# Kernel tuning notes

Measured on AMD Instinct MI355X. Metric: run time of the kernel, lower is better.

Reference implementation:

```python
import jax, jax.numpy as jnp
import numpy as np

N_HOPS = 6
NEG_INF = -1e30


def setup_inputs() -> dict:
    key = jax.random.key(0)
    ks = jax.random.split(key, 12)
    B, L, T, V, D, C = 64, 512, 8, 50000, 1024, 3
    context_ids = jax.random.randint(ks[0], (B, L), 0, V, dtype=jnp.int32)
    target_ids = jax.random.randint(ks[1], (B, T), 0, V, dtype=jnp.int32)
    context_len = jax.random.randint(ks[2], (B,), 256, L + 1, dtype=jnp.int32)
    target_len = jax.random.randint(ks[3], (B,), 2, T + 1, dtype=jnp.int32)
    target_offset = jax.random.randint(ks[4], (B,), 0, 256, dtype=jnp.int32)
    s = 0.02
    return {
        "context_ids": context_ids,
        "target_ids": target_ids,
        "context_len": context_len,
        "target_len": target_len,
        "target_offset": target_offset,
        "embedding_matrix": jax.random.normal(ks[5], (V, D), jnp.float32) * s,
        "W_lin": jax.random.normal(ks[6], (D, D), jnp.float32) * s,
        "b_lin": jax.random.normal(ks[7], (D,), jnp.float32) * s,
        "w_attn": jax.random.normal(ks[8], (2 * D, 1), jnp.float32) * s,
        "b_attn": jax.random.normal(ks[9], (1,), jnp.float32) * s,
        "W_out": jax.random.normal(ks[10], (D, C), jnp.float32) * s,
        "b_out": jax.random.normal(ks[11], (C,), jnp.float32) * s,
    }


def reference(context_ids, target_ids, context_len, target_len, target_offset,
              embedding_matrix, W_lin, b_lin, w_attn, b_attn, W_out, b_out):
    B, L = context_ids.shape
    T = target_ids.shape[1]

    pos = jnp.arange(L, dtype=jnp.int32)[None, :]            # [1,L]
    ctx_mask = pos < context_len[:, None]                    # [B,L] valid positions

    # location model 2: v_i = 1 - |i - target_offset| / seq_len, zeroed off-sequence
    dist = jnp.abs(pos - target_offset[:, None]).astype(jnp.float32)
    v_loc = (1.0 - dist / context_len[:, None].astype(jnp.float32))
    v_loc = jnp.where(ctx_mask, v_loc, 0.0)                  # [B,L]

    memory = embedding_matrix[context_ids]                   # [B,L,D]
    ext_memory = memory * v_loc[..., None]                   # [B,L,D] (loc-model-2 branch)

    # v_aspect: variable-length mean of target embeddings
    tgt_emb = embedding_matrix[target_ids]                   # [B,T,D]
    t_mask = (jnp.arange(T, dtype=jnp.int32)[None, :] < target_len[:, None])
    v_aspect = (tgt_emb * t_mask[..., None].astype(jnp.float32)).sum(axis=1)
    v_aspect = v_aspect / target_len[:, None].astype(jnp.float32)  # [B,D]

    vec = v_aspect
    for _ in range(N_HOPS):  # fixed hop count; linear + attn params shared (AUTO_REUSE)
        lin = vec @ W_lin + b_lin                            # [B,D]
        # content attention: tanh(W [m_i ; v] + b) scores
        s_mem = jnp.einsum('bld,dk->bl', ext_memory, w_attn[: ext_memory.shape[-1]])
        s_vec = vec @ w_attn[ext_memory.shape[-1]:]          # [B,1]
        scores = jnp.tanh(s_mem + s_vec + b_attn[0])         # [B,L]
        scores = jnp.where(ctx_mask, scores, NEG_INF)
        alpha = jax.nn.softmax(scores, axis=-1)              # [B,L]
        attn_out = jnp.einsum('bl,bld->bd', alpha, ext_memory)
        vec = attn_out + lin

    logits = vec @ W_out + b_out                             # [B,C]
    return logits
```

## Files before the change

kernel.cpp:

```cpp
#include <hip/hip_runtime.h>
#include <cstdint>


#define DD 1024
#define LL 512
#define BB 64
#define MTS 32

__global__ __launch_bounds__(256) void k_init(const float* __restrict__ w_attn,
                                              const float* __restrict__ W_out,
                                              float* __restrict__ Mt,
                                              float* __restrict__ Mc)
{
  int d = blockIdx.x * 256 + threadIdx.x;
  float w0 = w_attn[d];
  float u0 = w_attn[DD + d];
  Mt[d * MTS + 0] = w0; Mc[0 * DD + d] = w0;
  Mt[d * MTS + 1] = u0; Mc[1 * DD + d] = u0;
#pragma unroll
  for (int c = 0; c < 3; ++c) {
    float y = W_out[d * 3 + c];
    int col = 7 + 6 * c;
    Mt[d * MTS + col] = y; Mc[col * DD + d] = y;
  }
}

__global__ __launch_bounds__(256) void k_chain(const float* __restrict__ Wl,
                                               float* __restrict__ Mt,
                                               float* __restrict__ Mc,
                                               int i0, int i1, int i2, int i3,
                                               int o0, int o1, int o2, int o3)
{
  int tid = threadIdx.x;
  int wv = __builtin_amdgcn_readfirstlane(tid >> 6);
  int ln = tid & 63;
  int i = blockIdx.x * 4 + wv;
  const float* wrow = Wl + (size_t)i * DD;
  int c0 = i0 < 0 ? 0 : i0, c1 = i1 < 0 ? 0 : i1;
  int c2 = i2 < 0 ? 0 : i2, c3 = i3 < 0 ? 0 : i3;
  float s0 = 0.f, s1 = 0.f, s2 = 0.f, s3 = 0.f;
  for (int m = 0; m < 16; ++m) {
    int j = ln + m * 64;
    float w = wrow[j];
    s0 += w * Mc[c0 * DD + j];
    s1 += w * Mc[c1 * DD + j];
    s2 += w * Mc[c2 * DD + j];
    s3 += w * Mc[c3 * DD + j];
  }
#pragma unroll
  for (int m = 1; m < 64; m <<= 1) {
    s0 += __shfl_xor(s0, m, 64); s1 += __shfl_xor(s1, m, 64);
    s2 += __shfl_xor(s2, m, 64); s3 += __shfl_xor(s3, m, 64);
  }
  if (ln == 0) {
    if (o0 >= 0) { Mt[i * MTS + o0] = s0; Mc[o0 * DD + i] = s0; }
    if (o1 >= 0) { Mt[i * MTS + o1] = s1; Mc[o1 * DD + i] = s1; }
    if (o2 >= 0) { Mt[i * MTS + o2] = s2; Mc[o2 * DD + i] = s2; }
    if (o3 >= 0) { Mt[i * MTS + o3] = s3; Mc[o3 * DD + i] = s3; }
  }
}

__global__ __launch_bounds__(256, 2) void k_gemm(const int* __restrict__ ctx_ids,
                                                 const int* __restrict__ ctx_len,
                                                 const int* __restrict__ toff,
                                                 const float* __restrict__ emb,
                                                 const float* __restrict__ Mt,
                                                 float* __restrict__ Q)
{
  __shared__ float stag[4][64 * 33];
  __shared__ float qp[4][64][25];
  int tid = threadIdx.x;
  int kq = __builtin_amdgcn_readfirstlane(tid >> 6);
  int ln = tid & 63;
  int rowbase = blockIdx.x * 64;
  int myid = ctx_ids[rowbase + ln];
  const float* base[8];
#pragma unroll
  for (int ii = 0; ii < 8; ++ii) {
    int rid = __shfl(myid, ii * 8 + (ln >> 3), 64);
    base[ii] = emb + (size_t)rid * DD;
  }
  int p4 = (ln & 7) * 4;
  float* sw = stag[kq];
  int k0 = kq * 256;
  float acc[25];
#pragma unroll
  for (int j = 0; j < 25; ++j) acc[j] = 0.f;

  float4 buf[8];
#pragma unroll
  for (int ii = 0; ii < 8; ++ii)
    buf[ii] = *(const float4*)(base[ii] + k0 + p4);

  for (int ch = 0; ch < 8; ++ch) {
#pragma unroll
    for (int ii = 0; ii < 8; ++ii) {
      int r = ii * 8 + (ln >> 3);
      int a = r * 33 + p4;
      sw[a + 0] = buf[ii].x; sw[a + 1] = buf[ii].y;
      sw[a + 2] = buf[ii].z; sw[a + 3] = buf[ii].w;
    }
    if (ch < 7) {
      int kb = k0 + (ch + 1) * 32;
#pragma unroll
      for (int ii = 0; ii < 8; ++ii)
        buf[ii] = *(const float4*)(base[ii] + kb + p4);
    }
    __builtin_amdgcn_s_waitcnt(0xc07f);
    const float* mrow = Mt + (size_t)(k0 + ch * 32) * MTS;
#pragma unroll 4
    for (int kk = 0; kk < 32; ++kk) {
      float mv = sw[ln * 33 + kk];
#pragma unroll
      for (int j = 0; j < 25; ++j) acc[j] += mv * mrow[kk * MTS + j];
    }
  }
#pragma unroll
  for (int j = 0; j < 25; ++j) qp[kq][ln][j] = acc[j];
  __syncthreads();

  int b = rowbase >> 9;
  int l0 = rowbase & 511;
  int clen = ctx_len[b];
  int off = toff[b];
  float fclen = (float)clen;
  for (int i = tid; i < 1600; i += 256) {
    int j = i >> 6, r = i & 63;
    float s = qp[0][r][j] + qp[1][r][j] + qp[2][r][j] + qp[3][r][j];
    int l = l0 + r;
    float vl = (l < clen) ? (1.f - fabsf((float)(l - off)) / fclen) : 0.f;
    Q[((size_t)b * 25 + j) * LL + l] = s * vl;
  }
}

template <bool ISMAX>
__device__ __forceinline__ void breduce(float* v, int n, float* lds, int tid)
{
  int wv = __builtin_amdgcn_readfirstlane(tid >> 6);
  int ln = tid & 63;
  for (int q = 0; q < n; ++q) {
    float x = v[q];
#pragma unroll
    for (int m = 1; m < 64; m <<= 1) {
      float o = __shfl_xor(x, m, 64);
      x = ISMAX ? fmaxf(x, o) : x + o;
    }
    if (ln == 0) lds[q * 4 + wv] = x;
  }
  __syncthreads();
  for (int q = 0; q < n; ++q) {
    float a = lds[q * 4 + 0], b = lds[q * 4 + 1];
    float c = lds[q * 4 + 2], d = lds[q * 4 + 3];
    v[q] = ISMAX ? fmaxf(fmaxf(a, b), fmaxf(c, d)) : ((a + b) + (c + d));
  }
  __syncthreads();
}

__global__ __launch_bounds__(256) void k_hop(const int* __restrict__ tgt_ids,
                                             const int* __restrict__ tgt_len,
                                             const int* __restrict__ ctx_len,
                                             const float* __restrict__ emb,
                                             const float* __restrict__ b_lin,
                                             const float* __restrict__ b_attn,
                                             const float* __restrict__ b_out,
                                             const float* __restrict__ Mc,
                                             const float* __restrict__ Q,
                                             float* __restrict__ out)
{
  __shared__ float Qs[25 * LL];
  __shared__ float va[DD];
  __shared__ float red[36 * 4];
  int tid = threadIdx.x;
  int b = blockIdx.x;

  for (int i = tid; i < 25 * LL; i += 256) Qs[i] = Q[(size_t)b * (25 * LL) + i];

  int tl = tgt_len[b];
  float inv_tl = 1.f / (float)tl;
  for (int d = tid; d < DD; d += 256) {
    float s = 0.f;
#pragma unroll
    for (int t = 0; t < 8; ++t)
      if (t < tl) s += emb[(size_t)tgt_ids[b * 8 + t] * DD + d];
    va[d] = s * inv_tl;
  }
  __syncthreads();

  float p[32];
#pragma unroll
  for (int q = 0; q < 32; ++q) p[q] = 0.f;
  for (int d = tid; d < DD; d += 256) {
    float vad = va[d], bd = b_lin[d];
#pragma unroll
    for (int k = 0; k < 6; ++k) {
      float u = Mc[(1 + k) * DD + d];
      p[k] += vad * u;
      if (k < 5) p[9 + k] += bd * u;
    }
#pragma unroll
    for (int c = 0; c < 3; ++c) {
      p[6 + c] += vad * Mc[(25 + c) * DD + d];
#pragma unroll
      for (int k = 0; k < 6; ++k)
        p[14 + c * 6 + k] += bd * Mc[(7 + 6 * c + k) * DD + d];
    }
  }
  breduce<false>(p, 32, red, tid);

  float tcur[6], rc[3], beta[5], gam[18];
#pragma unroll
  for (int k = 0; k < 6; ++k) tcur[k] = p[k];
#pragma unroll
  for (int c = 0; c < 3; ++c) rc[c] = p[6 + c];
#pragma unroll
  for (int k = 0; k < 5; ++k) beta[k] = p[9 + k];
#pragma unroll
  for (int q = 0; q < 18; ++q) gam[q] = p[14 + q];

  int clen = ctx_len[b];
  float batt = b_attn[0];
  int l1 = tid, l2 = tid + 256;

  for (int h = 0; h < 6; ++h) {
    float s_h = tcur[0];
    float sc1 = -1e30f, sc2 = -1e30f;
    if (l1 < clen) sc1 = tanhf(Qs[l1] + s_h + batt);
    if (l2 < clen) sc2 = tanhf(Qs[l2] + s_h + batt);
    float mx = fmaxf(sc1, sc2);
    breduce<true>(&mx, 1, red, tid);

    float pe[9];
#pragma unroll
    for (int q = 0; q < 9; ++q) pe[q] = 0.f;
    int kd = 5 - h;
    if (l1 < clen) {
      float e = expf(sc1 - mx);
      pe[0] += e;
      for (int k = 0; k <= 4 - h; ++k) pe[1 + k] += e * Qs[(1 + k) * LL + l1];
#pragma unroll
      for (int c = 0; c < 3; ++c) pe[6 + c] += e * Qs[(7 + 6 * c + kd) * LL + l1];
    }
    if (l2 < clen) {
      float e = expf(sc2 - mx);
      pe[0] += e;
      for (int k = 0; k <= 4 - h; ++k) pe[1 + k] += e * Qs[(1 + k) * LL + l2];
#pragma unroll
      for (int c = 0; c < 3; ++c) pe[6 + c] += e * Qs[(7 + 6 * c + kd) * LL + l2];
    }
    breduce<false>(pe, 9, red, tid);

    float invS = 1.f / pe[0];
    for (int k = 0; k <= 4 - h; ++k)
      tcur[k] = pe[1 + k] * invS + tcur[k + 1] + beta[k];
#pragma unroll
    for (int c = 0; c < 3; ++c)
      rc[c] = pe[6 + c] * invS + rc[c] + gam[c * 6 + kd];
  }
  if (tid < 3) out[b * 3 + tid] = rc[tid] + b_out[tid];
}

extern "C" void kernel_launch(void* const* d_in, const int* in_sizes, int n_in,
                              void* d_out, int out_size, void* d_ws, size_t ws_size,
                              hipStream_t stream)
{
  const int*   ctx_ids = (const int*)d_in[0];
  const int*   tgt_ids = (const int*)d_in[1];
  const int*   ctx_len = (const int*)d_in[2];
  const int*   tgt_len = (const int*)d_in[3];
  const int*   toff    = (const int*)d_in[4];
  const float* emb     = (const float*)d_in[5];
  const float* Wl      = (const float*)d_in[6];
  const float* bl      = (const float*)d_in[7];
  const float* wat     = (const float*)d_in[8];
  const float* bat     = (const float*)d_in[9];
  const float* Wo      = (const float*)d_in[10];
  const float* bo      = (const float*)d_in[11];
  float* ws = (float*)d_ws;
  float* Mt = ws;
  float* Mc = ws + 32768;
  float* Q  = ws + 65536;
  float* outp = (float*)d_out;

  hipLaunchKernelGGL(k_init, dim3(4), dim3(256), 0, stream, wat, Wo, Mt, Mc);
  for (int s = 1; s <= 6; ++s) {
    int i0 = (s <= 5) ? s : -1;
    int o0 = (s <= 5) ? (1 + s) : -1;
    int i1 = 6 + s,  o1 = (s <= 5) ? (7 + s)  : 25;
    int i2 = 12 + s, o2 = (s <= 5) ? (13 + s) : 26;
    int i3 = 18 + s, o3 = (s <= 5) ? (19 + s) : 27;
    hipLaunchKernelGGL(k_chain, dim3(256), dim3(256), 0, stream,
                       Wl, Mt, Mc, i0, i1, i2, i3, o0, o1, o2, o3);
  }
  hipLaunchKernelGGL(k_gemm, dim3(512), dim3(256), 0, stream,
                     ctx_ids, ctx_len, toff, emb, Mt, Q);
  hipLaunchKernelGGL(k_hop, dim3(64), dim3(256), 0, stream,
                     tgt_ids, tgt_len, ctx_len, emb, bl, bat, bo, Mc, Q, outp);
}
```

Measured before the change: 363.4 us.

## Fuse init and chain launches into one cooperative kernel with grid syncs

Replaces the init kernel and six chained matvec launches with a single cooperative kernel that uses grid.sync between chain steps and keeps each W_lin row in registers across all steps. The target-embedding mean and the per-batch projection dot products move into this kernel, so the hop kernel only loads a 32-value vector per batch. The hop kernel now uses 512 threads, one per position, with float4 staging of Q into shared memory. This removes several launch gaps and repeated W_lin reads, at the cost of grid-wide barrier overhead and a dependence on cooperative launch support.

```diff
diff --git a/kernel.cpp b/kernel.cpp
--- a/kernel.cpp
+++ b/kernel.cpp
@@ -1,5 +1,8 @@
 #include <hip/hip_runtime.h>
+#include <hip/hip_cooperative_groups.h>
 #include <cstdint>
+
+namespace cg = cooperative_groups;
 
 
 #define DD 1024
@@ -7,56 +10,134 @@
 #define BB 64
 #define MTS 32
 
-__global__ __launch_bounds__(256) void k_init(const float* __restrict__ w_attn,
-                                              const float* __restrict__ W_out,
-                                              float* __restrict__ Mt,
-                                              float* __restrict__ Mc)
-{
-  int d = blockIdx.x * 256 + threadIdx.x;
-  float w0 = w_attn[d];
-  float u0 = w_attn[DD + d];
-  Mt[d * MTS + 0] = w0; Mc[0 * DD + d] = w0;
-  Mt[d * MTS + 1] = u0; Mc[1 * DD + d] = u0;
-#pragma unroll
-  for (int c = 0; c < 3; ++c) {
-    float y = W_out[d * 3 + c];
-    int col = 7 + 6 * c;
-    Mt[d * MTS + col] = y; Mc[col * DD + d] = y;
-  }
-}
-
-__global__ __launch_bounds__(256) void k_chain(const float* __restrict__ Wl,
-                                               float* __restrict__ Mt,
-                                               float* __restrict__ Mc,
-                                               int i0, int i1, int i2, int i3,
-                                               int o0, int o1, int o2, int o3)
-{
-  int tid = threadIdx.x;
+template <bool ISMAX, int NW>
+__device__ __forceinline__ void breduce(float* v, int n, float* lds, int tid)
+{
   int wv = __builtin_amdgcn_readfirstlane(tid >> 6);
   int ln = tid & 63;
-  int i = blockIdx.x * 4 + wv;
+  for (int q = 0; q < n; ++q) {
+    float x = v[q];
+#pragma unroll
+    for (int m = 1; m < 64; m <<= 1) {
+      float o = __shfl_xor(x, m, 64);
+      x = ISMAX ? fmaxf(x, o) : x + o;
+    }
+    if (ln == 0) lds[q * NW + wv] = x;
+  }
+  __syncthreads();
+  for (int q = 0; q < n; ++q) {
+    float r = lds[q * NW + 0];
+#pragma unroll
+    for (int w = 1; w < NW; ++w)
+      r = ISMAX ? fmaxf(r, lds[q * NW + w]) : r + lds[q * NW + w];
+    v[q] = r;
+  }
+  __syncthreads();
+}
+
+__global__ __launch_bounds__(256) void k_prep(const int* __restrict__ tgt_ids,
+                                              const int* __restrict__ tgt_len,
+                                              const float* __restrict__ emb,
+                                              const float* __restrict__ Wl,
+                                              const float* __restrict__ bl,
+                                              const float* __restrict__ wat,
+                                              const float* __restrict__ Wo,
+                                              float* __restrict__ Mt,
+                                              float* __restrict__ Mc,
+                                              float* __restrict__ va_ws,
+                                              float* __restrict__ pv)
+{
+  cg::grid_group grid = cg::this_grid();
+  __shared__ float red[32 * 4];
+  int tid = threadIdx.x;
+  int blk = blockIdx.x;
+  int gidx = blk * 256 + tid;
+
+  if (gidx < DD) {
+    int d = gidx;
+    float w0 = wat[d];
+    float u0 = wat[DD + d];
+    Mt[d * MTS + 0] = w0; Mc[0 * DD + d] = w0;
+    Mt[d * MTS + 1] = u0; Mc[1 * DD + d] = u0;
+#pragma unroll
+    for (int c = 0; c < 3; ++c) {
+      float y = Wo[d * 3 + c];
+      int col = 7 + 6 * c;
+      Mt[d * MTS + col] = y; Mc[col * DD + d] = y;
+    }
+  }
+  {
+    int b = gidx >> 10, d = gidx & (DD - 1);
+    int tl = tgt_len[b];
+    float s = 0.f;
+#pragma unroll
+    for (int t = 0; t < 8; ++t)
+      if (t < tl) s += emb[(size_t)tgt_ids[b * 8 + t] * DD + d];
+    va_ws[gidx] = s / (float)tl;
+  }
+  grid.sync();
+
+  int wv = tid >> 6, ln = tid & 63;
+  int i = blk * 4 + wv;
   const float* wrow = Wl + (size_t)i * DD;
-  int c0 = i0 < 0 ? 0 : i0, c1 = i1 < 0 ? 0 : i1;
-  int c2 = i2 < 0 ? 0 : i2, c3 = i3 < 0 ? 0 : i3;
-  float s0 = 0.f, s1 = 0.f, s2 = 0.f, s3 = 0.f;
-  for (int m = 0; m < 16; ++m) {
-    int j = ln + m * 64;
-    float w = wrow[j];
-    s0 += w * Mc[c0 * DD + j];
-    s1 += w * Mc[c1 * DD + j];
-    s2 += w * Mc[c2 * DD + j];
-    s3 += w * Mc[c3 * DD + j];
-  }
-#pragma unroll
-  for (int m = 1; m < 64; m <<= 1) {
-    s0 += __shfl_xor(s0, m, 64); s1 += __shfl_xor(s1, m, 64);
-    s2 += __shfl_xor(s2, m, 64); s3 += __shfl_xor(s3, m, 64);
-  }
-  if (ln == 0) {
-    if (o0 >= 0) { Mt[i * MTS + o0] = s0; Mc[o0 * DD + i] = s0; }
-    if (o1 >= 0) { Mt[i * MTS + o1] = s1; Mc[o1 * DD + i] = s1; }
-    if (o2 >= 0) { Mt[i * MTS + o2] = s2; Mc[o2 * DD + i] = s2; }
-    if (o3 >= 0) { Mt[i * MTS + o3] = s3; Mc[o3 * DD + i] = s3; }
+  float wreg[16];
+#pragma unroll
+  for (int m = 0; m < 16; ++m) wreg[m] = wrow[ln + m * 64];
+
+  for (int s = 1; s <= 6; ++s) {
+    int c0 = (s <= 5) ? s : 0;
+    int c1 = 6 + s, c2 = 12 + s, c3 = 18 + s;
+    float s0 = 0.f, s1 = 0.f, s2 = 0.f, s3 = 0.f;
+#pragma unroll
+    for (int m = 0; m < 16; ++m) {
+      int j = ln + m * 64;
+      float w = wreg[m];
+      s0 += w * Mc[c0 * DD + j];
+      s1 += w * Mc[c1 * DD + j];
+      s2 += w * Mc[c2 * DD + j];
+      s3 += w * Mc[c3 * DD + j];
+    }
+#pragma unroll
+    for (int m = 1; m < 64; m <<= 1) {
+      s0 += __shfl_xor(s0, m, 64); s1 += __shfl_xor(s1, m, 64);
+      s2 += __shfl_xor(s2, m, 64); s3 += __shfl_xor(s3, m, 64);
+    }
+    if (ln == 0) {
+      if (s <= 5) {
+        int o0 = 1 + s;  Mt[i * MTS + o0] = s0; Mc[o0 * DD + i] = s0;
+        int o1 = 7 + s;  Mt[i * MTS + o1] = s1; Mc[o1 * DD + i] = s1;
+        int o2 = 13 + s; Mt[i * MTS + o2] = s2; Mc[o2 * DD + i] = s2;
+        int o3 = 19 + s; Mt[i * MTS + o3] = s3; Mc[o3 * DD + i] = s3;
+      } else {
+        Mc[25 * DD + i] = s1; Mc[26 * DD + i] = s2; Mc[27 * DD + i] = s3;
+      }
+    }
+    grid.sync();
+  }
+
+  if (blk < BB) {
+    const float* va = va_ws + (size_t)blk * DD;
+    float p[32];
+#pragma unroll
+    for (int q = 0; q < 32; ++q) p[q] = 0.f;
+    for (int d = tid; d < DD; d += 256) {
+      float vad = va[d], bd = bl[d];
+#pragma unroll
+      for (int k = 0; k < 6; ++k) {
+        float u = Mc[(1 + k) * DD + d];
+        p[k] += vad * u;
+        if (k < 5) p[9 + k] += bd * u;
+      }
+#pragma unroll
+      for (int c = 0; c < 3; ++c) {
+        p[6 + c] += vad * Mc[(25 + c) * DD + d];
+#pragma unroll
+        for (int k = 0; k < 6; ++k)
+          p[14 + c * 6 + k] += bd * Mc[(7 + 6 * c + k) * DD + d];
+      }
+    }
+    breduce<false, 4>(p, 32, red, tid);
+    if (tid < 32) pv[blk * 32 + tid] = p[tid];
   }
 }
 
@@ -133,79 +214,27 @@
   }
 }
 
-template <bool ISMAX>
-__device__ __forceinline__ void breduce(float* v, int n, float* lds, int tid)
-{
-  int wv = __builtin_amdgcn_readfirstlane(tid >> 6);
-  int ln = tid & 63;
-  for (int q = 0; q < n; ++q) {
-    float x = v[q];
-#pragma unroll
-    for (int m = 1; m < 64; m <<= 1) {
-      float o = __shfl_xor(x, m, 64);
-      x = ISMAX ? fmaxf(x, o) : x + o;
-    }
-    if (ln == 0) lds[q * 4 + wv] = x;
-  }
-  __syncthreads();
-  for (int q = 0; q < n; ++q) {
-    float a = lds[q * 4 + 0], b = lds[q * 4 + 1];
-    float c = lds[q * 4 + 2], d = lds[q * 4 + 3];
-    v[q] = ISMAX ? fmaxf(fmaxf(a, b), fmaxf(c, d)) : ((a + b) + (c + d));
-  }
-  __syncthreads();
-}
-
-__global__ __launch_bounds__(256) void k_hop(const int* __restrict__ tgt_ids,
-                                             const int* __restrict__ tgt_len,
-                                             const int* __restrict__ ctx_len,
-                                             const float* __restrict__ emb,
-                                             const float* __restrict__ b_lin,
+__global__ __launch_bounds__(512) void k_hop(const int* __restrict__ ctx_len,
                                              const float* __restrict__ b_attn,
                                              const float* __restrict__ b_out,
-                                             const float* __restrict__ Mc,
+                                             const float* __restrict__ pv,
                                              const float* __restrict__ Q,
                                              float* __restrict__ out)
 {
   __shared__ float Qs[25 * LL];
-  __shared__ float va[DD];
-  __shared__ float red[36 * 4];
+  __shared__ float red[16 * 8];
   int tid = threadIdx.x;
   int b = blockIdx.x;
 
-  for (int i = tid; i < 25 * LL; i += 256) Qs[i] = Q[(size_t)b * (25 * LL) + i];
-
-  int tl = tgt_len[b];
-  float inv_tl = 1.f / (float)tl;
-  for (int d = tid; d < DD; d += 256) {
-    float s = 0.f;
-#pragma unroll
-    for (int t = 0; t < 8; ++t)
-      if (t < tl) s += emb[(size_t)tgt_ids[b * 8 + t] * DD + d];
-    va[d] = s * inv_tl;
-  }
-  __syncthreads();
+  {
+    const float4* src = (const float4*)(Q + (size_t)b * (25 * LL));
+    float4* dst = (float4*)Qs;
+    for (int i = tid; i < 25 * LL / 4; i += 512) dst[i] = src[i];
+  }
 
   float p[32];
 #pragma unroll
-  for (int q = 0; q < 32; ++q) p[q] = 0.f;
-  for (int d = tid; d < DD; d += 256) {
-    float vad = va[d], bd = b_lin[d];
-#pragma unroll
-    for (int k = 0; k < 6; ++k) {
-      float u = Mc[(1 + k) * DD + d];
-      p[k] += vad * u;
-      if (k < 5) p[9 + k] += bd * u;
-    }
-#pragma unroll
-    for (int c = 0; c < 3; ++c) {
-      p[6 + c] += vad * Mc[(25 + c) * DD + d];
-#pragma unroll
-      for (int k = 0; k < 6; ++k)
-        p[14 + c * 6 + k] += bd * Mc[(7 + 6 * c + k) * DD + d];
-    }
-  }
-  breduce<false>(p, 32, red, tid);
+  for (int q = 0; q < 32; ++q) p[q] = pv[b * 32 + q];
 
   float tcur[6], rc[3], beta[5], gam[18];
 #pragma unroll
@@ -219,35 +248,27 @@
 
   int clen = ctx_len[b];
   float batt = b_attn[0];
-  int l1 = tid, l2 = tid + 256;
+  bool act = tid < clen;
+  __syncthreads();
 
   for (int h = 0; h < 6; ++h) {
-    float s_h = tcur[0];
-    float sc1 = -1e30f, sc2 = -1e30f;
-    if (l1 < clen) sc1 = tanhf(Qs[l1] + s_h + batt);
-    if (l2 < clen) sc2 = tanhf(Qs[l2] + s_h + batt);
-    float mx = fmaxf(sc1, sc2);
-    breduce<true>(&mx, 1, red, tid);
+    float sc = -1e30f;
+    if (act) sc = tanhf(Qs[tid] + tcur[0] + batt);
+    float mx = sc;
+    breduce<true, 8>(&mx, 1, red, tid);
 
     float pe[9];
 #pragma unroll
     for (int q = 0; q < 9; ++q) pe[q] = 0.f;
     int kd = 5 - h;
-    if (l1 < clen) {
-      float e = expf(sc1 - mx);
-      pe[0] += e;
-      for (int k = 0; k <= 4 - h; ++k) pe[1 + k] += e * Qs[(1 + k) * LL + l1];
-#pragma unroll
-      for (int c = 0; c < 3; ++c) pe[6 + c] += e * Qs[(7 + 6 * c + kd) * LL + l1];
-    }
-    if (l2 < clen) {
-      float e = expf(sc2 - mx);
-      pe[0] += e;
-      for (int k = 0; k <= 4 - h; ++k) pe[1 + k] += e * Qs[(1 + k) * LL + l2];
-#pragma unroll
-      for (int c = 0; c < 3; ++c) pe[6 + c] += e * Qs[(7 + 6 * c + kd) * LL + l2];
-    }
-    breduce<false>(pe, 9, red, tid);
+    if (act) {
+      float e = expf(sc - mx);
+      pe[0] = e;
+      for (int k = 0; k <= 4 - h; ++k) pe[1 + k] = e * Qs[(1 + k) * LL + tid];
+#pragma unroll
+      for (int c = 0; c < 3; ++c) pe[6 + c] = e * Qs[(7 + 6 * c + kd) * LL + tid];
+    }
+    breduce<false, 8>(pe, 9, red, tid);
 
     float invS = 1.f / pe[0];
     for (int k = 0; k <= 4 - h; ++k)
@@ -279,20 +300,19 @@
   float* Mt = ws;
   float* Mc = ws + 32768;
   float* Q  = ws + 65536;
+  float* va = ws + 65536 + 819200;
+  float* pv = va + 65536;
   float* outp = (float*)d_out;
 
-  hipLaunchKernelGGL(k_init, dim3(4), dim3(256), 0, stream, wat, Wo, Mt, Mc);
-  for (int s = 1; s <= 6; ++s) {
-    int i0 = (s <= 5) ? s : -1;
-    int o0 = (s <= 5) ? (1 + s) : -1;
-    int i1 = 6 + s,  o1 = (s <= 5) ? (7 + s)  : 25;
-    int i2 = 12 + s, o2 = (s <= 5) ? (13 + s) : 26;
-    int i3 = 18 + s, o3 = (s <= 5) ? (19 + s) : 27;
-    hipLaunchKernelGGL(k_chain, dim3(256), dim3(256), 0, stream,
-                       Wl, Mt, Mc, i0, i1, i2, i3, o0, o1, o2, o3);
+  {
+    void* args[] = { (void*)&tgt_ids, (void*)&tgt_len, (void*)&emb, (void*)&Wl,
+                     (void*)&bl, (void*)&wat, (void*)&Wo,
+                     (void*)&Mt, (void*)&Mc, (void*)&va, (void*)&pv };
+    hipLaunchCooperativeKernel((const void*)k_prep, dim3(256), dim3(256),
+                               args, 0, stream);
   }
   hipLaunchKernelGGL(k_gemm, dim3(512), dim3(256), 0, stream,
                      ctx_ids, ctx_len, toff, emb, Mt, Q);
-  hipLaunchKernelGGL(k_hop, dim3(64), dim3(256), 0, stream,
-                     tgt_ids, tgt_len, ctx_len, emb, bl, bat, bo, Mc, Q, outp);
-}
+  hipLaunchKernelGGL(k_hop, dim3(64), dim3(512), 0, stream,
+                     ctx_len, bat, bo, pv, Q, outp);
+}
```

After: 572.3 us. 57.5% more time.

## Double-buffer gather loads in gemm and widen hop kernel to 512 threads

Applied to the files above, without the earlier changes.

The gemm kernel now prefetches two chunks of gathered embedding rows ahead instead of one, so more global load latency is hidden behind the LDS staging and FMA work, at the cost of more registers. The hop kernel moves to 512 threads with one context position per thread and uses float4 copies for the Q tile. It also drops the softmax max-reduction, since tanh bounds scores to [-1,1] and exp cannot overflow, which removes one block reduction and its barriers per hop. The reduction helper is templated on warp count so it can handle 8 waves.

```diff
diff --git a/kernel.cpp b/kernel.cpp
--- a/kernel.cpp
+++ b/kernel.cpp
@@ -87,24 +87,28 @@
 #pragma unroll
   for (int j = 0; j < 25; ++j) acc[j] = 0.f;
 
-  float4 buf[8];
+  float4 buf[2][8];
 #pragma unroll
   for (int ii = 0; ii < 8; ++ii)
-    buf[ii] = *(const float4*)(base[ii] + k0 + p4);
+    buf[0][ii] = *(const float4*)(base[ii] + k0 + p4);
+#pragma unroll
+  for (int ii = 0; ii < 8; ++ii)
+    buf[1][ii] = *(const float4*)(base[ii] + k0 + 32 + p4);
 
   for (int ch = 0; ch < 8; ++ch) {
+    int cur = ch & 1;
 #pragma unroll
     for (int ii = 0; ii < 8; ++ii) {
       int r = ii * 8 + (ln >> 3);
       int a = r * 33 + p4;
-      sw[a + 0] = buf[ii].x; sw[a + 1] = buf[ii].y;
-      sw[a + 2] = buf[ii].z; sw[a + 3] = buf[ii].w;
-    }
-    if (ch < 7) {
-      int kb = k0 + (ch + 1) * 32;
+      sw[a + 0] = buf[cur][ii].x; sw[a + 1] = buf[cur][ii].y;
+      sw[a + 2] = buf[cur][ii].z; sw[a + 3] = buf[cur][ii].w;
+    }
+    if (ch < 6) {
+      int kb = k0 + (ch + 2) * 32;
 #pragma unroll
       for (int ii = 0; ii < 8; ++ii)
-        buf[ii] = *(const float4*)(base[ii] + kb + p4);
+        buf[cur][ii] = *(const float4*)(base[ii] + kb + p4);
     }
     __builtin_amdgcn_s_waitcnt(0xc07f);
     const float* mrow = Mt + (size_t)(k0 + ch * 32) * MTS;
@@ -133,7 +137,7 @@
   }
 }
 
-template <bool ISMAX>
+template <bool ISMAX, int NW>
 __device__ __forceinline__ void breduce(float* v, int n, float* lds, int tid)
 {
   int wv = __builtin_amdgcn_readfirstlane(tid >> 6);
@@ -145,18 +149,20 @@
       float o = __shfl_xor(x, m, 64);
       x = ISMAX ? fmaxf(x, o) : x + o;
     }
-    if (ln == 0) lds[q * 4 + wv] = x;
+    if (ln == 0) lds[q * NW + wv] = x;
   }
   __syncthreads();
   for (int q = 0; q < n; ++q) {
-    float a = lds[q * 4 + 0], b = lds[q * 4 + 1];
-    float c = lds[q * 4 + 2], d = lds[q * 4 + 3];
-    v[q] = ISMAX ? fmaxf(fmaxf(a, b), fmaxf(c, d)) : ((a + b) + (c + d));
-  }
-  __syncthreads();
-}
-
-__global__ __launch_bounds__(256) void k_hop(const int* __restrict__ tgt_ids,
+    float r = lds[q * NW + 0];
+#pragma unroll
+    for (int w = 1; w < NW; ++w)
+      r = ISMAX ? fmaxf(r, lds[q * NW + w]) : r + lds[q * NW + w];
+    v[q] = r;
+  }
+  __syncthreads();
+}
+
+__global__ __launch_bounds__(512) void k_hop(const int* __restrict__ tgt_ids,
                                              const int* __restrict__ tgt_len,
                                              const int* __restrict__ ctx_len,
                                              const float* __restrict__ emb,
@@ -169,15 +175,19 @@
 {
   __shared__ float Qs[25 * LL];
   __shared__ float va[DD];
-  __shared__ float red[36 * 4];
+  __shared__ float red[32 * 8];
   int tid = threadIdx.x;
   int b = blockIdx.x;
 
-  for (int i = tid; i < 25 * LL; i += 256) Qs[i] = Q[(size_t)b * (25 * LL) + i];
+  {
+    const float4* src = (const float4*)(Q + (size_t)b * (25 * LL));
+    float4* dst = (float4*)Qs;
+    for (int i = tid; i < 25 * LL / 4; i += 512) dst[i] = src[i];
+  }
 
   int tl = tgt_len[b];
   float inv_tl = 1.f / (float)tl;
-  for (int d = tid; d < DD; d += 256) {
+  for (int d = tid; d < DD; d += 512) {
     float s = 0.f;
 #pragma unroll
     for (int t = 0; t < 8; ++t)
@@ -189,7 +199,7 @@
   float p[32];
 #pragma unroll
   for (int q = 0; q < 32; ++q) p[q] = 0.f;
-  for (int d = tid; d < DD; d += 256) {
+  for (int d = tid; d < DD; d += 512) {
     float vad = va[d], bd = b_lin[d];
 #pragma unroll
     for (int k = 0; k < 6; ++k) {
@@ -205,7 +215,7 @@
         p[14 + c * 6 + k] += bd * Mc[(7 + 6 * c + k) * DD + d];
     }
   }
-  breduce<false>(p, 32, red, tid);
+  breduce<false, 8>(p, 32, red, tid);
 
   float tcur[6], rc[3], beta[5], gam[18];
 #pragma unroll
@@ -219,35 +229,21 @@
 
   int clen = ctx_len[b];
   float batt = b_attn[0];
-  int l1 = tid, l2 = tid + 256;
+  bool act = tid < clen;
 
   for (int h = 0; h < 6; ++h) {
-    float s_h = tcur[0];
-    float sc1 = -1e30f, sc2 = -1e30f;
-    if (l1 < clen) sc1 = tanhf(Qs[l1] + s_h + batt);
-    if (l2 < clen) sc2 = tanhf(Qs[l2] + s_h + batt);
-    float mx = fmaxf(sc1, sc2);
-    breduce<true>(&mx, 1, red, tid);
-
     float pe[9];
 #pragma unroll
     for (int q = 0; q < 9; ++q) pe[q] = 0.f;
     int kd = 5 - h;
-    if (l1 < clen) {
-      float e = expf(sc1 - mx);
-      pe[0] += e;
-      for (int k = 0; k <= 4 - h; ++k) pe[1 + k] += e * Qs[(1 + k) * LL + l1];
-#pragma unroll
-      for (int c = 0; c < 3; ++c) pe[6 + c] += e * Qs[(7 + 6 * c + kd) * LL + l1];
-    }
-    if (l2 < clen) {
-      float e = expf(sc2 - mx);
-      pe[0] += e;
-      for (int k = 0; k <= 4 - h; ++k) pe[1 + k] += e * Qs[(1 + k) * LL + l2];
-#pragma unroll
-      for (int c = 0; c < 3; ++c) pe[6 + c] += e * Qs[(7 + 6 * c + kd) * LL + l2];
-    }
-    breduce<false>(pe, 9, red, tid);
+    if (act) {
+      float e = expf(tanhf(Qs[tid] + tcur[0] + batt));
+      pe[0] = e;
+      for (int k = 0; k <= 4 - h; ++k) pe[1 + k] = e * Qs[(1 + k) * LL + tid];
+#pragma unroll
+      for (int c = 0; c < 3; ++c) pe[6 + c] = e * Qs[(7 + 6 * c + kd) * LL + tid];
+    }
+    breduce<false, 8>(pe, 9, red, tid);
 
     float invS = 1.f / pe[0];
     for (int k = 0; k <= 4 - h; ++k)
@@ -293,6 +289,6 @@
   }
   hipLaunchKernelGGL(k_gemm, dim3(512), dim3(256), 0, stream,
                      ctx_ids, ctx_len, toff, emb, Mt, Q);
-  hipLaunchKernelGGL(k_hop, dim3(64), dim3(256), 0, stream,
+  hipLaunchKernelGGL(k_hop, dim3(64), dim3(512), 0, stream,
                      tgt_ids, tgt_len, ctx_len, emb, bl, bat, bo, Mc, Q, outp);
 }
```

Result: no change. 363.5 us (+0.0%).
